# Optimization experiments

Hardware: AMD Instinct MI355X
Metric: run time of the kernel (lower is better)

Reference implementation:

```python
import jax, jax.numpy as jnp
import numpy as np

B, S, H = 4, 1024, 1024
N, D = 16, 64  # num_heads, head_dim (key_dim = value_dim = H // N)
FF = 4096
EPS = 1e-5


def _glorot(key, shape):
    fan_in, fan_out = shape[-2], shape[-1]
    lim = np.sqrt(6.0 / (fan_in + fan_out))
    return jax.random.uniform(key, shape, jnp.float32, -lim, lim)


def setup_inputs() -> dict:
    key = jax.random.key(0)
    ks = jax.random.split(key, 32)
    inp = {
        "x": jax.random.normal(ks[0], (B, S, H), jnp.float32),
        # per-head complex Q/K projections (ComplexDense = two real Dense layers)
        "Wq_r": _glorot(ks[1], (N, H, D)), "Wq_i": _glorot(ks[2], (N, H, D)),
        "bq_r": jnp.zeros((N, D)), "bq_i": jnp.zeros((N, D)),
        "Wk_r": _glorot(ks[3], (N, H, D)), "Wk_i": _glorot(ks[4], (N, H, D)),
        "bk_r": jnp.zeros((N, D)), "bk_i": jnp.zeros((N, D)),
        # per-head real value projection
        "Wv": _glorot(ks[5], (N, H, D)), "bv": jnp.zeros((N, D)),
        # per-head positional interference weights (seq_len, key_dim)
        "pos_q_r": _glorot(ks[6], (N, S, D)), "pos_q_i": _glorot(ks[7], (N, S, D)),
        "pos_k_r": _glorot(ks[8], (N, S, D)), "pos_k_i": _glorot(ks[9], (N, S, D)),
        # multi-head output projection
        "Wo": _glorot(ks[10], (H, H)), "bo": jnp.zeros((H,)),
        # feedforward
        "W1": _glorot(ks[11], (H, FF)), "b1": jnp.zeros((FF,)),
        "W2": _glorot(ks[12], (FF, H)), "b2": jnp.zeros((H,)),
        # layer norms
        "g1": jnp.ones((H,)), "beta1": jnp.zeros((H,)),
        "g2": jnp.ones((H,)), "beta2": jnp.zeros((H,)),
    }
    return inp


def _layer_norm(x, g, b):
    mu = jnp.mean(x, axis=-1, keepdims=True)
    var = jnp.mean(jnp.square(x - mu), axis=-1, keepdims=True)
    return (x - mu) * jax.lax.rsqrt(var + EPS) * g + b


def reference(x, Wq_r, Wq_i, bq_r, bq_i, Wk_r, Wk_i, bk_r, bk_i, Wv, bv,
              pos_q_r, pos_q_i, pos_k_r, pos_k_i, Wo, bo, W1, b1, W2, b2,
              g1, beta1, g2, beta2):
    scale = 1.0 / np.sqrt(float(D))  # applied twice, as in the original
    # complex Q/K projections, all heads at once: [B,N,S,D]
    qr = jnp.einsum('bsh,nhd->bnsd', x, Wq_r) + bq_r[:, None, :]
    qi = jnp.einsum('bsh,nhd->bnsd', x, Wq_i) + bq_i[:, None, :]
    kr = jnp.einsum('bsh,nhd->bnsd', x, Wk_r) + bk_r[:, None, :]
    ki = jnp.einsum('bsh,nhd->bnsd', x, Wk_i) + bk_i[:, None, :]
    v = jnp.einsum('bsh,nhd->bnsd', x, Wv) + bv[:, None, :]
    # query scaled by 1/sqrt(D), then positional interference added (query and key)
    qr = qr * scale + pos_q_r[None]
    qi = qi * scale + pos_q_i[None]
    kr = kr + pos_k_r[None]
    ki = ki + pos_k_i[None]
    # real part of complex matmul q @ k^T (transpose_b, no conjugation), rescaled
    scores = (jnp.einsum('bnsd,bntd->bnst', qr, kr)
              - jnp.einsum('bnsd,bntd->bnst', qi, ki)) * scale
    probs = jax.nn.softmax(scores, axis=-1)  # temperature == 1.0 (use_temperature=False)
    heads = jnp.einsum('bnst,bntd->bnsd', probs, v)
    concat = heads.transpose(0, 2, 1, 3).reshape(x.shape[0], x.shape[1], N * D)
    attn_out = concat @ Wo + bo
    h1 = _layer_norm(x + attn_out, g1, beta1)
    ff = jax.nn.relu(h1 @ W1 + b1) @ W2 + b2
    return _layer_norm(h1 + ff, g2, beta2)
```

## Files before the change

### kernel.cpp

```cpp
#include <hip/hip_runtime.h>
#include <math.h>

typedef unsigned short u16;
typedef unsigned int   u32;
typedef __attribute__((ext_vector_type(8))) short short8;
typedef __attribute__((ext_vector_type(4))) float f32x4;
typedef __attribute__((ext_vector_type(4))) u16   us4;

constexpr int Bc = 4, Sc = 1024, Hc = 1024, Nc = 16, Dc = 64, FFc = 4096;

__device__ __forceinline__ u16 bfh(float v) {
  u32 u = __float_as_uint(v);
  return (u16)((u + 0x7FFFu + ((u >> 16) & 1u)) >> 16);
}
__device__ __forceinline__ void split2(float v, u16& h, u16& l) {
  h = bfh(v);
  l = bfh(v - __uint_as_float(((u32)h) << 16));
}

__device__ __forceinline__ void gl_lds16(const u16* g, u16* lds) {
  __builtin_amdgcn_global_load_lds(
      (const __attribute__((address_space(1))) void*)g,
      (__attribute__((address_space(3))) void*)lds, 16, 0, 0);
}

__device__ __forceinline__ f32x4 mfma_bf16(short8 a, short8 b, f32x4 c) {
  asm("v_mfma_f32_16x16x32_bf16 %0, %1, %2, %0" : "+v"(c) : "v"(a), "v"(b));
  return c;
}

__global__ __launch_bounds__(256)
void split_copy(const float* __restrict__ in, u16* __restrict__ oh,
                u16* __restrict__ ol, int n4) {
  int i = blockIdx.x * 256 + threadIdx.x;
  if (i >= n4) return;
  f32x4 v = ((const f32x4*)in)[i];
  us4 h4, l4;
#pragma unroll
  for (int c = 0; c < 4; ++c) { u16 h, l; split2(v[c], h, l); h4[c] = h; l4[c] = l; }
  ((us4*)oh)[i] = h4;
  ((us4*)ol)[i] = l4;
}

__global__ __launch_bounds__(256)
void transpose_split(const float* __restrict__ in, u16* __restrict__ oh,
                     u16* __restrict__ ol, int R, int C) {
  __shared__ float t[32][33];
  const int c0 = blockIdx.x * 32, r0 = blockIdx.y * 32;
  const int tx = threadIdx.x & 31, ty = threadIdx.x >> 5;
#pragma unroll
  for (int j = 0; j < 4; ++j)
    t[ty + 8 * j][tx] = in[(size_t)(r0 + ty + 8 * j) * C + c0 + tx];
  __syncthreads();
#pragma unroll
  for (int j = 0; j < 4; ++j) {
    float v = t[tx][ty + 8 * j];
    u16 h, l; split2(v, h, l);
    size_t o = (size_t)(c0 + ty + 8 * j) * R + r0 + tx;
    oh[o] = h; ol[o] = l;
  }
}

__global__ __launch_bounds__(256)
void conv_wproj(const float* __restrict__ Wqr, const float* __restrict__ Wqi,
                const float* __restrict__ Wkr, const float* __restrict__ Wki,
                const float* __restrict__ Wv,  u16* __restrict__ oh,
                u16* __restrict__ ol) {
  __shared__ float t[32][33];
  const int c0 = blockIdx.x * 32, k0 = blockIdx.y * 32;
  const int n = c0 / 320, w0 = c0 - n * 320;
  const int chunk = w0 >> 6, d0 = w0 & 63;
  const float* src; float sgn = 1.f;
  switch (chunk) {
    case 0: src = Wqr; break;
    case 1: src = Wqi; break;
    case 2: src = Wkr; break;
    case 3: src = Wki; sgn = -1.f; break;
    default: src = Wv; break;
  }
  const int tx = threadIdx.x & 31, ty = threadIdx.x >> 5;
#pragma unroll
  for (int j = 0; j < 4; ++j)
    t[ty + 8 * j][tx] = sgn * src[((size_t)n * 1024 + k0 + ty + 8 * j) * 64 + d0 + tx];
  __syncthreads();
#pragma unroll
  for (int j = 0; j < 4; ++j) {
    float v = t[tx][ty + 8 * j];
    u16 h, l; split2(v, h, l);
    size_t o = (size_t)(c0 + ty + 8 * j) * 1024 + k0 + tx;
    oh[o] = h; ol[o] = l;
  }
}

struct GemmP {
  const u16 *Ah, *Al, *Bh, *Bl;
  int N, K, lda;
  const float* bias;
  float* outf;
  float* outf1;
  u16 *oh, *ol;
  const float *bqr, *bqi, *bkr, *bki, *bv;
  const float *pqr, *pqi, *pkr, *pki;
  u16 *qh, *ql, *kh, *kl, *vth, *vtl;
};

template<int MODE>
__global__ __launch_bounds__(256, 4)
void mfma_gemm(GemmP p) {
  __shared__ __attribute__((aligned(16))) u16 sA[2][128 * 32];
  __shared__ __attribute__((aligned(16))) u16 sB[2][128 * 32];
  const int tid = threadIdx.x;
  const int w = tid >> 6, lane = tid & 63;
  const int wm = w >> 1, wn = w & 1;
  const int lrow = lane & 15, g = lane >> 4;
  const int bn = blockIdx.x * 128, bm = blockIdx.y * 128;
  const int K = p.K, lda = p.lda;
  const int koff = blockIdx.z * K;

  const int srow = lane >> 2;
  const int sseg = (lane & 3) ^ ((lane >> 3) & 3);
  const int rowl0 = w * 32, rowl1 = w * 32 + 16;

  f32x4 acc[4][4];
#pragma unroll
  for (int i = 0; i < 4; ++i)
#pragma unroll
    for (int j = 0; j < 4; ++j) acc[i][j] = (f32x4){0.f, 0.f, 0.f, 0.f};

  const int sw = (lrow >> 1) & 3;
  for (int kb = 0; kb < K; kb += 32) {
    const size_t ga0 = (size_t)(bm + rowl0 + srow) * lda + koff + kb + sseg * 8;
    const size_t gb0 = (size_t)(bn + rowl0 + srow) * lda + koff + kb + sseg * 8;
    const size_t ga1 = (size_t)(bm + rowl1 + srow) * lda + koff + kb + sseg * 8;
    const size_t gb1 = (size_t)(bn + rowl1 + srow) * lda + koff + kb + sseg * 8;
    gl_lds16(p.Ah + ga0, &sA[0][rowl0 * 32]);
    gl_lds16(p.Al + ga0, &sA[1][rowl0 * 32]);
    gl_lds16(p.Bh + gb0, &sB[0][rowl0 * 32]);
    gl_lds16(p.Bl + gb0, &sB[1][rowl0 * 32]);
    gl_lds16(p.Ah + ga1, &sA[0][rowl1 * 32]);
    gl_lds16(p.Al + ga1, &sA[1][rowl1 * 32]);
    gl_lds16(p.Bh + gb1, &sB[0][rowl1 * 32]);
    gl_lds16(p.Bl + gb1, &sB[1][rowl1 * 32]);
    __syncthreads();

    short8 bh[4], bl[4];
#pragma unroll
    for (int nf = 0; nf < 4; ++nf) {
      int idx = (wn * 64 + nf * 16 + lrow) * 32 + ((g ^ sw) * 8);
      bh[nf] = *(const short8*)&sB[0][idx];
      bl[nf] = *(const short8*)&sB[1][idx];
    }
#pragma unroll
    for (int mf = 0; mf < 4; ++mf) {
      int idx = (wm * 64 + mf * 16 + lrow) * 32 + ((g ^ sw) * 8);
      short8 ah = *(const short8*)&sA[0][idx];
      short8 al = *(const short8*)&sA[1][idx];
#pragma unroll
      for (int nf = 0; nf < 4; ++nf) {
        f32x4 a = acc[mf][nf];
        a = mfma_bf16(ah, bh[nf], a);
        a = mfma_bf16(ah, bl[nf], a);
        a = mfma_bf16(al, bh[nf], a);
        acc[mf][nf] = a;
      }
    }
    __syncthreads();
  }

#pragma unroll
  for (int nf = 0; nf < 4; ++nf) {
    const int c = bn + wn * 64 + nf * 16 + lrow;
    if (MODE == 0) {
      const int n = c / 320;
      const int wcol = c - n * 320;
      const int chunk = wcol >> 6, d = wcol & 63;
#pragma unroll
      for (int mf = 0; mf < 4; ++mf) {
        const int r0 = bm + wm * 64 + mf * 16 + g * 4;
        const int bb = r0 >> 10, s0 = r0 & 1023;
        const int head = bb * 16 + n;
        f32x4 a = acc[mf][nf];
        if (chunk == 4) {
          us4 hv, lv;
#pragma unroll
          for (int reg = 0; reg < 4; ++reg) {
            u16 hh, ll; split2(a[reg] + p.bv[n * 64 + d], hh, ll);
            hv[reg] = hh; lv[reg] = ll;
          }
          size_t o = ((size_t)head * 64 + d) * 1024 + s0;
          *(us4*)&p.vth[o] = hv;
          *(us4*)&p.vtl[o] = lv;
        } else {
#pragma unroll
          for (int reg = 0; reg < 4; ++reg) {
            const int s = s0 + reg;
            const size_t pidx = ((size_t)n * 1024 + s) * 64 + d;
            float val;
            u16 *dh, *dl;
            if (chunk == 0) {
              val = (a[reg] + p.bqr[n * 64 + d]) * 0.125f + p.pqr[pidx];
              dh = p.qh; dl = p.ql;
            } else if (chunk == 1) {
              val = (a[reg] + p.bqi[n * 64 + d]) * 0.125f + p.pqi[pidx];
              dh = p.qh; dl = p.ql;
            } else if (chunk == 2) {
              val = a[reg] + p.bkr[n * 64 + d] + p.pkr[pidx];
              dh = p.kh; dl = p.kl;
            } else {
              val = a[reg] - p.bki[n * 64 + d] - p.pki[pidx];
              dh = p.kh; dl = p.kl;
            }
            size_t o = ((size_t)head * 1024 + s) * 128 + (chunk & 1) * 64 + d;
            u16 hh, ll; split2(val, hh, ll);
            dh[o] = hh; dl[o] = ll;
          }
        }
      }
    } else if (MODE == 1) {
      float* outp = blockIdx.z ? p.outf1 : p.outf;
#pragma unroll
      for (int mf = 0; mf < 4; ++mf) {
        const int r0 = bm + wm * 64 + mf * 16 + g * 4;
        f32x4 a = acc[mf][nf];
#pragma unroll
        for (int reg = 0; reg < 4; ++reg)
          outp[(size_t)(r0 + reg) * p.N + c] = a[reg];
      }
    } else {
      const float bb = p.bias[c];
#pragma unroll
      for (int mf = 0; mf < 4; ++mf) {
        const int r0 = bm + wm * 64 + mf * 16 + g * 4;
        f32x4 a = acc[mf][nf];
#pragma unroll
        for (int reg = 0; reg < 4; ++reg) {
          const size_t o = (size_t)(r0 + reg) * p.N + c;
          float v = fmaxf(a[reg] + bb, 0.f);
          u16 h, l; split2(v, h, l);
          p.oh[o] = h; p.ol[o] = l;
        }
      }
    }
  }
}

__global__ __launch_bounds__(256)
void attn_mfma(const u16* __restrict__ qh, const u16* __restrict__ ql,
               const u16* __restrict__ kh, const u16* __restrict__ kl,
               const u16* __restrict__ vth, const u16* __restrict__ vtl,
               u16* __restrict__ ch, u16* __restrict__ cl) {
  __shared__ __attribute__((aligned(16))) u16 ksh[64 * 128];
  __shared__ __attribute__((aligned(16))) u16 ksl[64 * 128];
  __shared__ __attribute__((aligned(16))) u16 vsh[64 * 64];
  __shared__ __attribute__((aligned(16))) u16 vsl[64 * 64];
  __shared__ __attribute__((aligned(16))) u16 ps[4][2][16 * 64];

  const int tid = threadIdx.x;
  const int w = tid >> 6, lane = tid & 63;
  const int lo16 = lane & 15, hi4 = lane >> 4;
  const int n = blockIdx.y, b = blockIdx.z;
  const int head = b * Nc + n;
  const int q0 = blockIdx.x * 64;
  const u16* qbh = qh + (size_t)head * 1024 * 128;
  const u16* qbl = ql + (size_t)head * 1024 * 128;
  const u16* kbh = kh + (size_t)head * 1024 * 128;
  const u16* kbl = kl + (size_t)head * 1024 * 128;
  const u16* vbh = vth + (size_t)head * 64 * 1024;
  const u16* vbl = vtl + (size_t)head * 64 * 1024;

  {
    const int ri = lane >> 4, slot = lane & 15;
#pragma unroll
    for (int i = 0; i < 4; ++i) {
      const int row = w * 16 + i * 4 + ri;
      const int sg = slot ^ (row & 7);
      const size_t src = (size_t)(q0 + row) * 128 + sg * 8;
      gl_lds16(qbh + src, &ksh[(w * 16 + i * 4) * 128]);
      gl_lds16(qbl + src, &ksl[(w * 16 + i * 4) * 128]);
    }
  }
  __syncthreads();
  short8 qf[2][4];
  {
    const int qrow = w * 16 + lo16;
#pragma unroll
    for (int ks = 0; ks < 4; ++ks) {
      const int addr = qrow * 128 + (((ks * 4 + hi4) ^ (qrow & 7)) * 8);
      qf[0][ks] = *(const short8*)&ksh[addr];
      qf[1][ks] = *(const short8*)&ksl[addr];
    }
  }
  __syncthreads();

  f32x4 acc_o[4];
  float m_[4], l_[4];
#pragma unroll
  for (int i = 0; i < 4; ++i) {
    acc_o[i] = (f32x4){0.f, 0.f, 0.f, 0.f};
    m_[i] = -1e30f; l_[i] = 0.f;
  }

  for (int kt = 0; kt < 16; ++kt) {
    const int k0 = kt * 64;
    {
      const int ri = lane >> 4, slot = lane & 15;
#pragma unroll
      for (int i = 0; i < 4; ++i) {
        const int row = w * 16 + i * 4 + ri;
        const int sg = slot ^ (row & 7);
        const size_t src = (size_t)(k0 + row) * 128 + sg * 8;
        gl_lds16(kbh + src, &ksh[(w * 16 + i * 4) * 128]);
        gl_lds16(kbl + src, &ksl[(w * 16 + i * 4) * 128]);
      }
      const int di = lane >> 3, vslot = lane & 7;
#pragma unroll
      for (int i = 0; i < 2; ++i) {
        const int d = w * 16 + i * 8 + di;
        const int sg = vslot ^ (d & 7);
        const size_t src = (size_t)d * 1024 + k0 + sg * 8;
        gl_lds16(vbh + src, &vsh[(w * 16 + i * 8) * 64]);
        gl_lds16(vbl + src, &vsl[(w * 16 + i * 8) * 64]);
      }
    }
    __syncthreads();

    f32x4 sc[4];
#pragma unroll
    for (int cg = 0; cg < 4; ++cg) sc[cg] = (f32x4){0.f, 0.f, 0.f, 0.f};
#pragma unroll
    for (int cg = 0; cg < 4; ++cg) {
      const int key = cg * 16 + lo16;
#pragma unroll
      for (int ks = 0; ks < 4; ++ks) {
        const int addr = key * 128 + (((ks * 4 + hi4) ^ (key & 7)) * 8);
        short8 bhf = *(const short8*)&ksh[addr];
        short8 blf = *(const short8*)&ksl[addr];
        f32x4 a = sc[cg];
        a = mfma_bf16(qf[0][ks], bhf, a);
        a = mfma_bf16(qf[0][ks], blf, a);
        a = mfma_bf16(qf[1][ks], bhf, a);
        sc[cg] = a;
      }
    }
    float pv[4][4];
#pragma unroll
    for (int reg = 0; reg < 4; ++reg) {
      float mx = fmaxf(fmaxf(sc[0][reg], sc[1][reg]),
                       fmaxf(sc[2][reg], sc[3][reg])) * 0.125f;
#pragma unroll
      for (int off = 1; off < 16; off <<= 1) mx = fmaxf(mx, __shfl_xor(mx, off));
      const float mn = fmaxf(m_[reg], mx);
      const float corr = __expf(m_[reg] - mn);
      m_[reg] = mn;
      float sum = 0.f;
#pragma unroll
      for (int cg = 0; cg < 4; ++cg) {
        float pe = __expf(sc[cg][reg] * 0.125f - mn);
        pv[cg][reg] = pe; sum += pe;
      }
#pragma unroll
      for (int off = 1; off < 16; off <<= 1) sum += __shfl_xor(sum, off);
      l_[reg] = l_[reg] * corr + sum;
#pragma unroll
      for (int cg = 0; cg < 4; ++cg) acc_o[cg][reg] *= corr;
    }
#pragma unroll
    for (int cg = 0; cg < 4; ++cg) {
      const int key = cg * 16 + lo16;
#pragma unroll
      for (int reg = 0; reg < 4; ++reg) {
        const int row = hi4 * 4 + reg;
        const int pa = row * 64 + (((key >> 3) ^ (row >> 1)) * 8) + (key & 7);
        u16 hh, ll; split2(pv[cg][reg], hh, ll);
        ps[w][0][pa] = hh;
        ps[w][1][pa] = ll;
      }
    }
    short8 pah[2], pal[2];
#pragma unroll
    for (int ks2 = 0; ks2 < 2; ++ks2) {
      const int addr = lo16 * 64 + (((ks2 * 4 + hi4) ^ (lo16 >> 1)) * 8);
      pah[ks2] = *(const short8*)&ps[w][0][addr];
      pal[ks2] = *(const short8*)&ps[w][1][addr];
    }
#pragma unroll
    for (int cg = 0; cg < 4; ++cg) {
      const int d = cg * 16 + lo16;
#pragma unroll
      for (int ks2 = 0; ks2 < 2; ++ks2) {
        const int addr = d * 64 + (((ks2 * 4 + hi4) ^ (d & 7)) * 8);
        short8 vhf = *(const short8*)&vsh[addr];
        short8 vlf = *(const short8*)&vsl[addr];
        f32x4 a = acc_o[cg];
        a = mfma_bf16(pah[ks2], vhf, a);
        a = mfma_bf16(pah[ks2], vlf, a);
        a = mfma_bf16(pal[ks2], vhf, a);
        acc_o[cg] = a;
      }
    }
    __syncthreads();
  }

  float inv[4];
#pragma unroll
  for (int reg = 0; reg < 4; ++reg) inv[reg] = 1.f / l_[reg];
#pragma unroll
  for (int cg = 0; cg < 4; ++cg) {
#pragma unroll
    for (int reg = 0; reg < 4; ++reg) {
      const int qrow = q0 + w * 16 + hi4 * 4 + reg;
      const size_t o = ((size_t)b * Sc + qrow) * 1024 + n * 64 + cg * 16 + lo16;
      u16 hh, ll; split2(acc_o[cg][reg] * inv[reg], hh, ll);
      ch[o] = hh; cl[o] = ll;
    }
  }
}

template<bool SPLIT>
__global__ __launch_bounds__(256)
void ln_fuse(const float* __restrict__ P0, const float* __restrict__ P1,
             const float* __restrict__ resid, const float* __restrict__ bias,
             const float* __restrict__ gam, const float* __restrict__ bet,
             float* __restrict__ out, u16* __restrict__ oh,
             u16* __restrict__ ol) {
  const int row = blockIdx.x, t = threadIdx.x;
  const size_t base = (size_t)row * 1024;
  f32x4 v = ((const f32x4*)(P0 + base))[t];
  f32x4 p1 = ((const f32x4*)(P1 + base))[t];
  f32x4 rr = ((const f32x4*)(resid + base))[t];
  f32x4 bb = ((const f32x4*)bias)[t];
#pragma unroll
  for (int c = 0; c < 4; ++c) v[c] += p1[c] + rr[c] + bb[c];
  float s = v[0] + v[1] + v[2] + v[3];
  float q = v[0] * v[0] + v[1] * v[1] + v[2] * v[2] + v[3] * v[3];
#pragma unroll
  for (int off = 1; off < 64; off <<= 1) {
    s += __shfl_xor(s, off);
    q += __shfl_xor(q, off);
  }
  __shared__ float red[8];
  int wv = t >> 6, lnid = t & 63;
  if (lnid == 0) { red[wv] = s; red[4 + wv] = q; }
  __syncthreads();
  s = red[0] + red[1] + red[2] + red[3];
  q = red[4] + red[5] + red[6] + red[7];
  float mu = s * (1.f / 1024.f);
  float var = q * (1.f / 1024.f) - mu * mu;
  float ri = rsqrtf(var + 1e-5f);
  f32x4 g4 = ((const f32x4*)gam)[t];
  f32x4 b4 = ((const f32x4*)bet)[t];
  f32x4 o;
#pragma unroll
  for (int c = 0; c < 4; ++c) o[c] = (v[c] - mu) * ri * g4[c] + b4[c];
  ((f32x4*)(out + base))[t] = o;
  if (SPLIT) {
    us4 h4, l4;
#pragma unroll
    for (int c = 0; c < 4; ++c) {
      u16 hh, ll; split2(o[c], hh, ll);
      h4[c] = hh; l4[c] = ll;
    }
    *(us4*)&oh[base + t * 4] = h4;
    *(us4*)&ol[base + t * 4] = l4;
  }
}

extern "C" void kernel_launch(void* const* d_in, const int* in_sizes, int n_in,
                              void* d_out, int out_size, void* d_ws, size_t ws_size,
                              hipStream_t stream) {
  const float* x    = (const float*)d_in[0];
  const float* Wq_r = (const float*)d_in[1];
  const float* Wq_i = (const float*)d_in[2];
  const float* bq_r = (const float*)d_in[3];
  const float* bq_i = (const float*)d_in[4];
  const float* Wk_r = (const float*)d_in[5];
  const float* Wk_i = (const float*)d_in[6];
  const float* bk_r = (const float*)d_in[7];
  const float* bk_i = (const float*)d_in[8];
  const float* Wv   = (const float*)d_in[9];
  const float* bv   = (const float*)d_in[10];
  const float* pq_r = (const float*)d_in[11];
  const float* pq_i = (const float*)d_in[12];
  const float* pk_r = (const float*)d_in[13];
  const float* pk_i = (const float*)d_in[14];
  const float* Wo   = (const float*)d_in[15];
  const float* bo   = (const float*)d_in[16];
  const float* W1   = (const float*)d_in[17];
  const float* b1   = (const float*)d_in[18];
  const float* W2   = (const float*)d_in[19];
  const float* b2   = (const float*)d_in[20];
  const float* g1   = (const float*)d_in[21];
  const float* be1  = (const float*)d_in[22];
  const float* g2   = (const float*)d_in[23];
  const float* be2  = (const float*)d_in[24];

  char* Wb = (char*)d_ws;
  const size_t MB = (size_t)1 << 20;
  u16* qch = (u16*)(Wb + 0 * MB);
  u16* qcl = (u16*)(Wb + 16 * MB);
  u16* kch = (u16*)(Wb + 32 * MB);
  u16* kcl = (u16*)(Wb + 48 * MB);
  u16* vth = (u16*)(Wb + 64 * MB);
  u16* vtl = (u16*)(Wb + 72 * MB);
  u16* xh  = (u16*)(Wb + 80 * MB);
  u16* xl  = (u16*)(Wb + 88 * MB);
  u16* ch  = xh; u16* cl = xl;
  u16* w2h = xh; u16* w2l = xl;
  u16* wph = (u16*)(Wb + 96 * MB);
  u16* wpl = (u16*)(Wb + 106 * MB);
  u16* w1h = (u16*)(Wb + 96 * MB);
  u16* w1l = (u16*)(Wb + 104 * MB);
  u16* woh = (u16*)(Wb + 112 * MB);
  u16* wol = (u16*)(Wb + 114 * MB);
  float* h1 = (float*)(Wb + 120 * MB);
  u16* h1h = (u16*)(Wb + 136 * MB);
  u16* h1l = (u16*)(Wb + 144 * MB);
  float* P0 = (float*)(Wb + 0 * MB);
  float* P1 = (float*)(Wb + 16 * MB);
  u16* ffh = (u16*)(Wb + 0 * MB);
  u16* ffl = (u16*)(Wb + 32 * MB);
  float* Q0 = (float*)(Wb + 64 * MB);
  float* Q1 = (float*)(Wb + 96 * MB);

  split_copy<<<4096, 256, 0, stream>>>(x, xh, xl, (Bc * Sc * Hc) / 4);
  conv_wproj<<<dim3(160, 32), 256, 0, stream>>>(Wq_r, Wq_i, Wk_r, Wk_i, Wv, wph, wpl);
  GemmP pp = {};
  pp.Ah = xh; pp.Al = xl; pp.Bh = wph; pp.Bl = wpl;
  pp.N = 5120; pp.K = 1024; pp.lda = 1024;
  pp.bqr = bq_r; pp.bqi = bq_i; pp.bkr = bk_r; pp.bki = bk_i; pp.bv = bv;
  pp.pqr = pq_r; pp.pqi = pq_i; pp.pkr = pk_r; pp.pki = pk_i;
  pp.qh = qch; pp.ql = qcl; pp.kh = kch; pp.kl = kcl; pp.vth = vth; pp.vtl = vtl;
  mfma_gemm<0><<<dim3(40, 32), 256, 0, stream>>>(pp);
  transpose_split<<<dim3(128, 32), 256, 0, stream>>>(W1, w1h, w1l, 1024, 4096);
  transpose_split<<<dim3(32, 32), 256, 0, stream>>>(Wo, woh, wol, 1024, 1024);
  attn_mfma<<<dim3(16, 16, 4), 256, 0, stream>>>(qch, qcl, kch, kcl, vth, vtl, ch, cl);
  GemmP po = {};
  po.Ah = ch; po.Al = cl; po.Bh = woh; po.Bl = wol;
  po.N = 1024; po.K = 512; po.lda = 1024;
  po.outf = P0; po.outf1 = P1;
  mfma_gemm<1><<<dim3(8, 32, 2), 256, 0, stream>>>(po);
  transpose_split<<<dim3(32, 128), 256, 0, stream>>>(W2, w2h, w2l, 4096, 1024);
  ln_fuse<true><<<4096, 256, 0, stream>>>(P0, P1, x, bo, g1, be1, h1, h1h, h1l);
  GemmP p1 = {};
  p1.Ah = h1h; p1.Al = h1l; p1.Bh = w1h; p1.Bl = w1l;
  p1.N = 4096; p1.K = 1024; p1.lda = 1024;
  p1.bias = b1; p1.oh = ffh; p1.ol = ffl;
  mfma_gemm<2><<<dim3(32, 32), 256, 0, stream>>>(p1);
  GemmP p2 = {};
  p2.Ah = ffh; p2.Al = ffl; p2.Bh = w2h; p2.Bl = w2l;
  p2.N = 1024; p2.K = 2048; p2.lda = 4096;
  p2.outf = Q0; p2.outf1 = Q1;
  mfma_gemm<1><<<dim3(8, 32, 2), 256, 0, stream>>>(p2);
  ln_fuse<false><<<4096, 256, 0, stream>>>(Q0, Q1, h1, b2, g2, be2,
                                           (float*)d_out, nullptr, nullptr);
}
```

Before: 827.3 us.

## Double-buffer GEMM LDS tiles to overlap global loads with MFMA compute

Doubles the shared-memory A/B tile buffers in the split-bf16 MFMA GEMM and prefetches the next K-slice into the alternate buffer while computing on the current one. Explicit vmcnt waits and raw barriers replace __syncthreads so the in-flight prefetch is not drained early. This is meant to hide global-to-LDS load latency behind matrix math. The cost is twice the LDS per block and a lower occupancy hint in launch bounds (4 to 2), so fewer blocks per CU can hide latency.

```diff
diff --git a/kernel.cpp b/kernel.cpp
--- a/kernel.cpp
+++ b/kernel.cpp
@@ -105,10 +105,10 @@
 };
 
 template<int MODE>
-__global__ __launch_bounds__(256, 4)
+__global__ __launch_bounds__(256, 2)
 void mfma_gemm(GemmP p) {
-  __shared__ __attribute__((aligned(16))) u16 sA[2][128 * 32];
-  __shared__ __attribute__((aligned(16))) u16 sB[2][128 * 32];
+  __shared__ __attribute__((aligned(16))) u16 sA[2][2][128 * 32];
+  __shared__ __attribute__((aligned(16))) u16 sB[2][2][128 * 32];
   const int tid = threadIdx.x;
   const int w = tid >> 6, lane = tid & 63;
   const int wm = w >> 1, wn = w & 1;
@@ -127,34 +127,46 @@
 #pragma unroll
     for (int j = 0; j < 4; ++j) acc[i][j] = (f32x4){0.f, 0.f, 0.f, 0.f};
 
-  const int sw = (lrow >> 1) & 3;
-  for (int kb = 0; kb < K; kb += 32) {
+  auto stage = [&](int buf, int kb) {
     const size_t ga0 = (size_t)(bm + rowl0 + srow) * lda + koff + kb + sseg * 8;
     const size_t gb0 = (size_t)(bn + rowl0 + srow) * lda + koff + kb + sseg * 8;
     const size_t ga1 = (size_t)(bm + rowl1 + srow) * lda + koff + kb + sseg * 8;
     const size_t gb1 = (size_t)(bn + rowl1 + srow) * lda + koff + kb + sseg * 8;
-    gl_lds16(p.Ah + ga0, &sA[0][rowl0 * 32]);
-    gl_lds16(p.Al + ga0, &sA[1][rowl0 * 32]);
-    gl_lds16(p.Bh + gb0, &sB[0][rowl0 * 32]);
-    gl_lds16(p.Bl + gb0, &sB[1][rowl0 * 32]);
-    gl_lds16(p.Ah + ga1, &sA[0][rowl1 * 32]);
-    gl_lds16(p.Al + ga1, &sA[1][rowl1 * 32]);
-    gl_lds16(p.Bh + gb1, &sB[0][rowl1 * 32]);
-    gl_lds16(p.Bl + gb1, &sB[1][rowl1 * 32]);
-    __syncthreads();
+    gl_lds16(p.Ah + ga0, &sA[buf][0][rowl0 * 32]);
+    gl_lds16(p.Al + ga0, &sA[buf][1][rowl0 * 32]);
+    gl_lds16(p.Bh + gb0, &sB[buf][0][rowl0 * 32]);
+    gl_lds16(p.Bl + gb0, &sB[buf][1][rowl0 * 32]);
+    gl_lds16(p.Ah + ga1, &sA[buf][0][rowl1 * 32]);
+    gl_lds16(p.Al + ga1, &sA[buf][1][rowl1 * 32]);
+    gl_lds16(p.Bh + gb1, &sB[buf][0][rowl1 * 32]);
+    gl_lds16(p.Bl + gb1, &sB[buf][1][rowl1 * 32]);
+  };
+
+  const int sw = (lrow >> 1) & 3;
+  stage(0, 0);
+  int cur = 0;
+  for (int kb = 0; kb < K; kb += 32) {
+    if (kb + 32 < K) {
+      stage(cur ^ 1, kb + 32);
+      asm volatile("s_waitcnt vmcnt(8)" ::: "memory");
+    } else {
+      asm volatile("s_waitcnt vmcnt(0)" ::: "memory");
+    }
+    __builtin_amdgcn_s_barrier();
+    __builtin_amdgcn_sched_barrier(0);
 
     short8 bh[4], bl[4];
 #pragma unroll
     for (int nf = 0; nf < 4; ++nf) {
       int idx = (wn * 64 + nf * 16 + lrow) * 32 + ((g ^ sw) * 8);
-      bh[nf] = *(const short8*)&sB[0][idx];
-      bl[nf] = *(const short8*)&sB[1][idx];
+      bh[nf] = *(const short8*)&sB[cur][0][idx];
+      bl[nf] = *(const short8*)&sB[cur][1][idx];
     }
 #pragma unroll
     for (int mf = 0; mf < 4; ++mf) {
       int idx = (wm * 64 + mf * 16 + lrow) * 32 + ((g ^ sw) * 8);
-      short8 ah = *(const short8*)&sA[0][idx];
-      short8 al = *(const short8*)&sA[1][idx];
+      short8 ah = *(const short8*)&sA[cur][0][idx];
+      short8 al = *(const short8*)&sA[cur][1][idx];
 #pragma unroll
       for (int nf = 0; nf < 4; ++nf) {
         f32x4 a = acc[mf][nf];
@@ -164,7 +176,10 @@
         acc[mf][nf] = a;
       }
     }
-    __syncthreads();
+    asm volatile("s_waitcnt lgkmcnt(0)" ::: "memory");
+    __builtin_amdgcn_s_barrier();
+    __builtin_amdgcn_sched_barrier(0);
+    cur ^= 1;
   }
 
 #pragma unroll
```

Result: slower. 856.4 us (+3.5%).
